# Performance work log

Hardware: AMD Instinct MI355X
Metric: run time of the kernel (lower is better)

## Reference

```python
import jax, jax.numpy as jnp
import numpy as np

RADIUS = 1.0
NSAMPLE = 8
GROUPS = 8
EPS = 1e-5


def setup_inputs() -> dict:
    key = jax.random.key(0)
    ks = jax.random.split(key, 8)
    b, n_p, dim, C = 4, 4096, 128, 64
    coords = jax.random.normal(ks[0], (b, n_p, 3), jnp.float32)
    xyz2 = jax.random.normal(ks[1], (b, n_p, 3), jnp.float32)
    fmap1 = jax.random.normal(ks[2], (b, dim, n_p), jnp.float32)
    fmap2 = jax.random.normal(ks[3], (b, dim, n_p), jnp.float32)
    conv_w = jax.random.normal(ks[4], (C, 4), jnp.float32) * 0.1
    conv_b = jnp.zeros((C,), jnp.float32)
    gn_gamma = jnp.ones((C,), jnp.float32)
    gn_beta = jnp.zeros((C,), jnp.float32)
    prelu_a = jnp.full((1,), 0.25, jnp.float32)
    out_w = jax.random.normal(ks[5], (C, C), jnp.float32) * 0.1
    out_b = jnp.zeros((C,), jnp.float32)
    return {"coords": coords, "xyz2": xyz2, "fmap1": fmap1, "fmap2": fmap2,
            "conv_w": conv_w, "conv_b": conv_b, "gn_gamma": gn_gamma,
            "gn_beta": gn_beta, "prelu_a": prelu_a, "out_w": out_w, "out_b": out_b}


def ball_query(xyz2, coords, radius, nsample):
    # first-nsample points of xyz2 within `radius` of each query in coords,
    # padded with the first valid index (0 if none) -- matches PointNet++ ball query.
    n = xyz2.shape[1]
    d2 = jnp.sum((coords[:, :, None, :] - xyz2[:, None, :, :]) ** 2, axis=-1)  # [b,m,n]
    j = jnp.arange(n, dtype=jnp.float32)
    score = jnp.where(d2 < radius * radius, -j, -float(n))  # larger score = earlier valid idx
    vals, _ = jax.lax.top_k(score, nsample)  # [b,m,nsample]
    valid = vals > -float(n)
    idx = (-vals).astype(jnp.int32)
    first = jnp.where(valid[..., :1], idx[..., :1], 0)
    return jnp.where(valid, idx, first)  # [b,m,nsample]


def reference(coords, xyz2, fmap1, fmap2, conv_w, conv_b, gn_gamma, gn_beta, prelu_a, out_w, out_b):
    b, n_p, _ = coords.shape
    dim = fmap1.shape[1]
    # corr = fmap1^T fmap2 / sqrt(dim): [b, n_p, n_p]
    corr = jnp.einsum('bdn,bdm->bnm', fmap1, fmap2) / jnp.sqrt(jnp.float32(dim))
    idx = ball_query(xyz2, coords, RADIUS, NSAMPLE)  # [b,n_p,nsample]
    # grouped_xyz: xyz2[idx] - coords -> [b, 3, n_p, nsample]
    gathered = jax.vmap(lambda pts, ind: pts[ind])(xyz2, idx)  # [b,n_p,ns,3]
    grouped_xyz = jnp.transpose(gathered - coords[:, :, None, :], (0, 3, 1, 2))
    # corr gather along source dim
    cur_corr = jnp.take_along_axis(corr, idx, axis=2)[:, None]  # [b,1,n_p,ns]
    feat = jnp.concatenate([cur_corr, grouped_xyz], axis=1)  # [b,4,n_p,ns]
    # 1x1 Conv2d
    x = jnp.einsum('oc,bcns->bons', conv_w, feat) + conv_b[None, :, None, None]
    # GroupNorm(8, 64)
    C = x.shape[1]
    xg = x.reshape(b, GROUPS, C // GROUPS, n_p, NSAMPLE)
    mu = jnp.mean(xg, axis=(2, 3, 4), keepdims=True)
    var = jnp.var(xg, axis=(2, 3, 4), keepdims=True)
    xg = (xg - mu) * jax.lax.rsqrt(var + EPS)
    x = xg.reshape(b, C, n_p, NSAMPLE) * gn_gamma[None, :, None, None] + gn_beta[None, :, None, None]
    # PReLU (single shared slope)
    x = jnp.where(x >= 0, x, prelu_a[0] * x)
    # max over neighbors
    x = jnp.max(x, axis=3)  # [b,64,n_p]
    # 1x1 Conv1d out
    return jnp.einsum('oc,bcn->bon', out_w, x) + out_b[None, :, None]
```

## Files before the change

kernel.cpp:

```cpp
#include <hip/hip_runtime.h>
#include <hip/hip_cooperative_groups.h>
#include <math.h>

namespace cg = cooperative_groups;

#define B 4
#define NP 4096
#define DIM 128
#define CCH 64
#define NS 8

struct SM {
  float4 fs4[128];
  int sidx[128];
  float4 ow4[1024];
  float cw[256];
  float cb[64], ob[64];
  union {
    float tile[128][35];
    struct { float As[16 * 132]; float red[4][14]; } k2;
    struct {
      float4 vs4[256];
      float Av[64], Bv[64], red2[8][14], Sm[14], SxA[64], SxxA[64];
    } k3;
  } u;
};

__global__ __launch_bounds__(256, 4) void fused_all(
    const float* __restrict__ coords, const float* __restrict__ xyz2,
    const float* __restrict__ f1, const float* __restrict__ f2,
    const float* __restrict__ conv_w, const float* __restrict__ conv_b,
    const float* __restrict__ gamma, const float* __restrict__ beta,
    const float* __restrict__ prelu, const float* __restrict__ out_w,
    const float* __restrict__ out_b, float* __restrict__ out,
    float* __restrict__ f2T, float* __restrict__ parts, int useT) {
  cg::grid_group grid = cg::this_grid();
  __shared__ SM sm;
  int blk = blockIdx.x;
  int t = threadIdx.x;
  int bq = (blk & 7) >> 1;
  int chunk = ((blk >> 3) << 1) | (blk & 1);
  int m0 = chunk * 16;

  if (useT) {
    int b = blk >> 8;
    int n0 = (blk & 255) * 16;
    const float* s = f2 + (size_t)b * DIM * NP;
    float* dd = f2T + (size_t)b * NP * DIM;
#pragma unroll
    for (int it = 0; it < 2; ++it) {
      int f = t + it * 256;
      int d = f >> 2, ng = f & 3;
      float4 v = *(const float4*)&s[(size_t)d * NP + n0 + ng * 4];
      *(float4*)&sm.u.tile[d][ng * 4 + (d >> 5)] = v;
    }
    __syncthreads();
#pragma unroll
    for (int it = 0; it < 2; ++it) {
      int f = t + it * 256;
      int n = f >> 5, dg = f & 31;
      int ar = dg >> 3;
      float4 w;
      w.x = sm.u.tile[dg * 4 + 0][n + ar];
      w.y = sm.u.tile[dg * 4 + 1][n + ar];
      w.z = sm.u.tile[dg * 4 + 2][n + ar];
      w.w = sm.u.tile[dg * 4 + 3][n + ar];
      *(float4*)&dd[(size_t)(n0 + n) * DIM + dg * 4] = w;
    }
  }

  {
    int wv = t >> 6, lane = t & 63;
    const float* xz = xyz2 + (size_t)bq * NP * 3;
    float cx[4], cy[4], cz[4];
#pragma unroll
    for (int qi = 0; qi < 4; ++qi) {
      const float* cp = coords + ((size_t)bq * NP + m0 + wv * 4 + qi) * 3;
      cx[qi] = cp[0]; cy[qi] = cp[1]; cz[qi] = cp[2];
    }
    int cnt[4] = {0, 0, 0, 0};
    int first[4] = {0, 0, 0, 0};
    int j0 = lane * 3;
    float ax = xz[j0], ay = xz[j0 + 1], az = xz[j0 + 2];
    int j1 = (64 + lane) * 3;
    float bx = xz[j1], by = xz[j1 + 1], bz = xz[j1 + 2];
#pragma unroll 1
    for (int c = 0; c < 64; c += 2) {
      int c2 = (c + 2 < 64) ? c + 2 : 63;
      int c3 = (c + 3 < 64) ? c + 3 : 63;
      int jn2 = (c2 * 64 + lane) * 3, jn3 = (c3 * 64 + lane) * 3;
      float nax = xz[jn2], nay = xz[jn2 + 1], naz = xz[jn2 + 2];
      float nbx = xz[jn3], nby = xz[jn3 + 1], nbz = xz[jn3 + 2];
#pragma unroll
      for (int qi = 0; qi < 4; ++qi) {
        if (cnt[qi] < NS) {
          float dx = __fsub_rn(cx[qi], ax);
          float dy = __fsub_rn(cy[qi], ay);
          float dz = __fsub_rn(cz[qi], az);
          float d2 = __fadd_rn(__fadd_rn(__fmul_rn(dx, dx), __fmul_rn(dy, dy)),
                               __fmul_rn(dz, dz));
          bool hit = d2 < 1.0f;
          unsigned long long mk = __ballot(hit);
          if (mk) {
            int rank = cnt[qi] + __popcll(mk & ((1ull << lane) - 1ull));
            if (hit && rank < NS)
              sm.sidx[(wv * 4 + qi) * NS + rank] = c * 64 + lane;
            if (cnt[qi] == 0) first[qi] = c * 64 + (__ffsll(mk) - 1);
            cnt[qi] += __popcll(mk);
          }
        }
      }
      if ((cnt[0] >= NS) & (cnt[1] >= NS) & (cnt[2] >= NS) & (cnt[3] >= NS))
        break;
#pragma unroll
      for (int qi = 0; qi < 4; ++qi) {
        if (cnt[qi] < NS) {
          float dx = __fsub_rn(cx[qi], bx);
          float dy = __fsub_rn(cy[qi], by);
          float dz = __fsub_rn(cz[qi], bz);
          float d2 = __fadd_rn(__fadd_rn(__fmul_rn(dx, dx), __fmul_rn(dy, dy)),
                               __fmul_rn(dz, dz));
          bool hit = d2 < 1.0f;
          unsigned long long mk = __ballot(hit);
          if (mk) {
            int rank = cnt[qi] + __popcll(mk & ((1ull << lane) - 1ull));
            if (hit && rank < NS)
              sm.sidx[(wv * 4 + qi) * NS + rank] = (c + 1) * 64 + lane;
            if (cnt[qi] == 0) first[qi] = (c + 1) * 64 + (__ffsll(mk) - 1);
            cnt[qi] += __popcll(mk);
          }
        }
      }
      if ((cnt[0] >= NS) & (cnt[1] >= NS) & (cnt[2] >= NS) & (cnt[3] >= NS))
        break;
      ax = nax; ay = nay; az = naz;
      bx = nbx; by = nby; bz = nbz;
    }
#pragma unroll
    for (int qi = 0; qi < 4; ++qi) {
      if (lane < NS && lane >= cnt[qi])
        sm.sidx[(wv * 4 + qi) * NS + lane] = first[qi];
    }
  }

  {
    const float4* src = (const float4*)out_w;
#pragma unroll
    for (int k = 0; k < 4; ++k) {
      int i4 = t + k * 256;
      int oo = i4 >> 4, gg = i4 & 15;
      sm.ow4[oo * 16 + (gg ^ ((oo >> 2) & 7))] = src[i4];
    }
    sm.cw[t] = conv_w[t];
    if (t < 64) {
      sm.cb[t] = conv_b[t];
      sm.ob[t] = out_b[t];
    }
  }

  grid.sync();

  {
    auto& k2 = sm.u.k2;
    int b = bq;
    int g = t >> 3;
    int l = t & 7;
    float pm[14];
#pragma unroll
    for (int k = 0; k < 14; ++k) pm[k] = 0.f;

    if (useT) {
      int id0 = sm.sidx[g], id1 = sm.sidx[32 + g];
      int id2 = sm.sidx[64 + g], id3 = sm.sidx[96 + g];
      const float4* br0 = (const float4*)(f2T + ((size_t)b * NP + id0) * DIM) + l;
      const float4* br1 = (const float4*)(f2T + ((size_t)b * NP + id1) * DIM) + l;
      const float4* br2 = (const float4*)(f2T + ((size_t)b * NP + id2) * DIM) + l;
      const float4* br3 = (const float4*)(f2T + ((size_t)b * NP + id3) * DIM) + l;
      float4 y00 = br0[0], y01 = br0[8], y02 = br0[16], y03 = br0[24];
      float4 y10 = br1[0], y11 = br1[8], y12 = br1[16], y13 = br1[24];
      const float* xq0 = xyz2 + ((size_t)b * NP + id0) * 3;
      const float* xq1 = xyz2 + ((size_t)b * NP + id1) * 3;
      float x0x = xq0[0], x0y = xq0[1], x0z = xq0[2];
      float x1x = xq1[0], x1y = xq1[1], x1z = xq1[2];

#pragma unroll
      for (int pass = 0; pass < 2; ++pass) {
        int d = pass * 64 + (t >> 2);
        int j4 = t & 3;
        float4 v = *(const float4*)&f1[(size_t)(b * DIM + d) * NP + m0 + j4 * 4];
        k2.As[(j4 * 4 + 0) * 132 + d] = v.x;
        k2.As[(j4 * 4 + 1) * 132 + d] = v.y;
        k2.As[(j4 * 4 + 2) * 132 + d] = v.z;
        k2.As[(j4 * 4 + 3) * 132 + d] = v.w;
      }
      __syncthreads();
      float4 y20 = br2[0], y21 = br2[8], y22 = br2[16], y23 = br2[24];
      float4 y30 = br3[0], y31 = br3[8], y32 = br3[16], y33 = br3[24];
      const float* xq2 = xyz2 + ((size_t)b * NP + id2) * 3;
      const float* xq3 = xyz2 + ((size_t)b * NP + id3) * 3;
      float x2x = xq2[0], x2y = xq2[1], x2z = xq2[2];
      float x3x = xq3[0], x3y = xq3[1], x3z = xq3[2];

#define DO_R(r, ya, yb, yc, yd, nxx, nxy, nxz)                                 \
      {                                                                        \
        int pi = (r) * 32 + g;                                                 \
        int m = pi >> 3;                                                       \
        const float4* arow = (const float4*)&k2.As[m * 132] + l;               \
        float4 a0 = arow[0], a1 = arow[8], a2 = arow[16], a3 = arow[24];       \
        float acc = a0.x * ya.x + a0.y * ya.y + a0.z * ya.z + a0.w * ya.w +    \
                    a1.x * yb.x + a1.y * yb.y + a1.z * yb.z + a1.w * yb.w +    \
                    a2.x * yc.x + a2.y * yc.y + a2.z * yc.z + a2.w * yc.w +    \
                    a3.x * yd.x + a3.y * yd.y + a3.z * yd.z + a3.w * yd.w;     \
        acc += __shfl_xor(acc, 1);                                             \
        acc += __shfl_xor(acc, 2);                                             \
        acc += __shfl_xor(acc, 4);                                             \
        float corr = acc * 0.08838834764831843f;                               \
        const float* cpq = coords + ((size_t)b * NP + m0 + m) * 3;             \
        float dx = nxx - cpq[0], dy = nxy - cpq[1], dz = nxz - cpq[2];         \
        if (l == 0) {                                                          \
          float4 fv;                                                           \
          fv.x = corr; fv.y = dx; fv.z = dy; fv.w = dz;                        \
          sm.fs4[pi] = fv;                                                     \
        }                                                                      \
        pm[0] += corr; pm[1] += dx; pm[2] += dy; pm[3] += dz;                  \
        pm[4] += corr * corr; pm[5] += corr * dx; pm[6] += corr * dy;          \
        pm[7] += corr * dz; pm[8] += dx * dx; pm[9] += dx * dy;                \
        pm[10] += dx * dz; pm[11] += dy * dy; pm[12] += dy * dz;               \
        pm[13] += dz * dz;                                                     \
      }
      DO_R(0, y00, y01, y02, y03, x0x, x0y, x0z)
      DO_R(1, y10, y11, y12, y13, x1x, x1y, x1z)
      DO_R(2, y20, y21, y22, y23, x2x, x2y, x2z)
      DO_R(3, y30, y31, y32, y33, x3x, x3y, x3z)
#undef DO_R
    } else {
      __syncthreads();
      int idv[4];
#pragma unroll
      for (int r = 0; r < 4; ++r) idv[r] = sm.sidx[r * 32 + g];
#pragma unroll
      for (int r = 0; r < 4; ++r) {
        int pi = r * 32 + g;
        int m = pi >> 3;
        int id = idv[r];
        float acc = 0.f;
#pragma unroll
        for (int k = 0; k < 4; ++k) {
#pragma unroll
          for (int c = 0; c < 4; ++c) {
            int d = (l + 8 * k) * 4 + c;
            acc += f1[(size_t)(b * DIM + d) * NP + m0 + m] *
                   f2[(size_t)(b * DIM + d) * NP + id];
          }
        }
        acc += __shfl_xor(acc, 1);
        acc += __shfl_xor(acc, 2);
        acc += __shfl_xor(acc, 4);
        float corr = acc * 0.08838834764831843f;
        const float* cpq = coords + ((size_t)b * NP + m0 + m) * 3;
        const float* xp = xyz2 + ((size_t)b * NP + id) * 3;
        float dx = xp[0] - cpq[0], dy = xp[1] - cpq[1], dz = xp[2] - cpq[2];
        if (l == 0) {
          float4 fv;
          fv.x = corr; fv.y = dx; fv.z = dy; fv.w = dz;
          sm.fs4[pi] = fv;
        }
        pm[0] += corr; pm[1] += dx; pm[2] += dy; pm[3] += dz;
        pm[4] += corr * corr; pm[5] += corr * dx; pm[6] += corr * dy;
        pm[7] += corr * dz; pm[8] += dx * dx; pm[9] += dx * dy;
        pm[10] += dx * dz; pm[11] += dy * dy; pm[12] += dy * dz;
        pm[13] += dz * dz;
      }
    }

#pragma unroll
    for (int k = 0; k < 14; ++k) {
      float v = pm[k];
#pragma unroll
      for (int off = 32; off; off >>= 1) v += __shfl_xor(v, off);
      pm[k] = v;
    }
    int lane = t & 63, wvv = t >> 6;
    if (lane == 0) {
#pragma unroll
      for (int k = 0; k < 14; ++k) k2.red[wvv][k] = pm[k];
    }
    __syncthreads();
    if (t < 14) {
      float ssum = (k2.red[0][t] + k2.red[1][t] + k2.red[2][t] + k2.red[3][t]) * 0.125f;
      parts[((size_t)bq * 256 + chunk) * 14 + t] = ssum;
    }
  }

  grid.sync();

  {
    auto& kb = sm.u.k3;
    int b = bq;
    int n0 = m0;
    if (t < 112) {
      int k = t % 14, jg = t / 14;
      float s = 0.f;
      const float* pp = parts + ((size_t)b * 256 + jg * 32) * 14 + k;
#pragma unroll 8
      for (int j = 0; j < 32; ++j) s += pp[j * 14];
      kb.red2[jg][k] = s;
    }
    float alpha = prelu[0];
    __syncthreads();
    if (t < 14) {
      float s = 0.f;
#pragma unroll
      for (int jg = 0; jg < 8; ++jg) s += kb.red2[jg][t];
      kb.Sm[t] = s;
    }
    __syncthreads();
    if (t < 64) {
      int o = t;
      float w0 = sm.cw[o * 4 + 0], w1 = sm.cw[o * 4 + 1];
      float w2 = sm.cw[o * 4 + 2], w3 = sm.cw[o * 4 + 3];
      float bo = sm.cb[o];
      const float cnt = (float)(NP * NS);
      float wS1 = w0 * kb.Sm[0] + w1 * kb.Sm[1] + w2 * kb.Sm[2] + w3 * kb.Sm[3];
      float q = w0 * w0 * kb.Sm[4] + w1 * w1 * kb.Sm[8] + w2 * w2 * kb.Sm[11] +
                w3 * w3 * kb.Sm[13] +
                2.f * (w0 * w1 * kb.Sm[5] + w0 * w2 * kb.Sm[6] + w0 * w3 * kb.Sm[7] +
                       w1 * w2 * kb.Sm[9] + w1 * w3 * kb.Sm[10] + w2 * w3 * kb.Sm[12]);
      kb.SxA[o] = wS1 + bo * cnt;
      kb.SxxA[o] = q + 2.f * bo * wS1 + bo * bo * cnt;
    }
    __syncthreads();
    if (t < 64) {
      int o = t, g = o >> 3;
      const float cnt = (float)(NP * NS);
      float sm_ = 0.f, s2 = 0.f;
#pragma unroll
      for (int k = 0; k < 8; ++k) {
        sm_ += kb.SxA[g * 8 + k];
        s2 += kb.SxxA[g * 8 + k];
      }
      float mean = sm_ / (cnt * 8.f);
      float e2 = s2 / (cnt * 8.f);
      float var = e2 - mean * mean;
      float inv = rsqrtf(var + 1e-5f);
      float A = gamma[o] * inv;
      kb.Av[o] = A;
      kb.Bv[o] = beta[o] - mean * A;
    }
    __syncthreads();

    {
      int o = t & 63;
      int pw = t >> 6;
      float w0 = sm.cw[o * 4 + 0], w1 = sm.cw[o * 4 + 1];
      float w2 = sm.cw[o * 4 + 2], w3 = sm.cw[o * 4 + 3];
      float A = kb.Av[o], Bc = kb.Bv[o], bb = sm.cb[o];
      float* vsf = (float*)kb.vs4;
#pragma unroll
      for (int i = 0; i < 4; ++i) {
        int p = pw * 4 + i;
        float mx = -INFINITY;
#pragma unroll
        for (int s = 0; s < NS; ++s) {
          float4 f = sm.fs4[p * 8 + s];
          float x = fmaf(w0, f.x, fmaf(w1, f.y, fmaf(w2, f.z, fmaf(w3, f.w, bb))));
          float y = fmaf(A, x, Bc);
          y = (y >= 0.f) ? y : alpha * y;
          mx = fmaxf(mx, y);
        }
        vsf[(p * 16 + ((o >> 2) ^ ((p >> 2) & 7))) * 4 + (o & 3)] = mx;
      }
    }
    __syncthreads();

    {
      int ti = t >> 3;
      int tj = t & 7;
      float acc[2][2];
#pragma unroll
      for (int oi = 0; oi < 2; ++oi)
#pragma unroll
        for (int pj = 0; pj < 2; ++pj) acc[oi][pj] = 0.f;
#pragma unroll
      for (int g = 0; g < 16; ++g) {
        float4 vv[2], ww[2];
#pragma unroll
        for (int pj = 0; pj < 2; ++pj) {
          int p = tj * 2 + pj;
          vv[pj] = kb.vs4[p * 16 + (g ^ ((p >> 2) & 7))];
        }
#pragma unroll
        for (int oi = 0; oi < 2; ++oi) {
          int oo = ti * 2 + oi;
          ww[oi] = sm.ow4[oo * 16 + (g ^ ((oo >> 2) & 7))];
        }
#pragma unroll
        for (int oi = 0; oi < 2; ++oi)
#pragma unroll
          for (int pj = 0; pj < 2; ++pj) {
            acc[oi][pj] = fmaf(ww[oi].x, vv[pj].x, acc[oi][pj]);
            acc[oi][pj] = fmaf(ww[oi].y, vv[pj].y, acc[oi][pj]);
            acc[oi][pj] = fmaf(ww[oi].z, vv[pj].z, acc[oi][pj]);
            acc[oi][pj] = fmaf(ww[oi].w, vv[pj].w, acc[oi][pj]);
          }
      }
#pragma unroll
      for (int oi = 0; oi < 2; ++oi) {
        int oo = ti * 2 + oi;
        float bb = sm.ob[oo];
        float2 r;
        r.x = acc[oi][0] + bb;
        r.y = acc[oi][1] + bb;
        *(float2*)&out[((size_t)b * CCH + oo) * NP + n0 + tj * 2] = r;
      }
    }
  }
}

__global__ __launch_bounds__(256) void kA_bq_transpose(
    const float* __restrict__ coords, const float* __restrict__ xyz2,
    int* __restrict__ idxb, const float* __restrict__ f2,
    float* __restrict__ o2) {
  int blk = blockIdx.x;
  int t = threadIdx.x;
  __shared__ float tile[128][33];
  if (blk < B * NP) {
    int b = blk >> 12, m = blk & (NP - 1);
    int wv = t >> 6, lane = t & 63;
    const float* cp = coords + ((size_t)b * NP + m) * 3;
    float cx = cp[0], cy = cp[1], cz = cp[2];
    const float* xz = xyz2 + (size_t)b * NP * 3;
    int base = wv * 1024;
    int j0 = (base + lane) * 3;
    float px = xz[j0], py = xz[j0 + 1], pz = xz[j0 + 2];
    int cnt = 0, myidx = 0;
    for (int c = 0; c < 16 && cnt < NS; ++c) {
      int cn = (c < 15) ? c + 1 : 15;
      int jn = (base + cn * 64 + lane) * 3;
      float nx = xz[jn], ny = xz[jn + 1], nz = xz[jn + 2];
      float dx = __fsub_rn(cx, px);
      float dy = __fsub_rn(cy, py);
      float dz = __fsub_rn(cz, pz);
      float d2 = __fadd_rn(__fadd_rn(__fmul_rn(dx, dx), __fmul_rn(dy, dy)),
                           __fmul_rn(dz, dz));
      unsigned long long mk = __ballot(d2 < 1.0f);
      while (mk && cnt < NS) {
        int bpos = __ffsll(mk) - 1;
        int jf = base + c * 64 + bpos;
        if (lane == cnt) myidx = jf;
        ++cnt;
        mk &= mk - 1;
      }
      px = nx; py = ny; pz = nz;
    }
    __shared__ int sidx[4][NS];
    __shared__ int scnt[4];
    if (lane < NS) sidx[wv][lane] = myidx;
    if (lane == 0) scnt[wv] = cnt;
    __syncthreads();
    if (t < NS) {
      int c0 = scnt[0], c1 = scnt[1], c2 = scnt[2], c3 = scnt[3];
      int total = c0 + c1 + c2 + c3;
      int v;
      if (t < c0) v = sidx[0][t];
      else if (t < c0 + c1) v = sidx[1][t - c0];
      else if (t < c0 + c1 + c2) v = sidx[2][t - c0 - c1];
      else if (t < total) v = sidx[3][t - c0 - c1 - c2];
      else v = (c0 > 0) ? sidx[0][0]
             : (c1 > 0) ? sidx[1][0]
             : (c2 > 0) ? sidx[2][0]
             : (c3 > 0) ? sidx[3][0] : 0;
      idxb[((size_t)b * NP + m) * NS + t] = v;
    }
  } else {
    int tb = blk - B * NP;
    int b = tb >> 7;
    int n0 = (tb & 127) * 32;
    const float* s = f2 + (size_t)b * DIM * NP;
    float* d = o2 + (size_t)b * NP * DIM;
    int dr = t >> 3;
    int ng = t & 7;
#pragma unroll
    for (int k = 0; k < 4; ++k) {
      int dd = dr + 32 * k;
      float4 v = *(const float4*)&s[(size_t)dd * NP + n0 + ng * 4];
      tile[dd][ng * 4 + 0] = v.x;
      tile[dd][ng * 4 + 1] = v.y;
      tile[dd][ng * 4 + 2] = v.z;
      tile[dd][ng * 4 + 3] = v.w;
    }
    __syncthreads();
    int n = t >> 3;
#pragma unroll
    for (int k = 0; k < 4; ++k) {
      int d0 = (t & 7) * 4 + 32 * k;
      float4 w;
      w.x = tile[d0 + 0][n];
      w.y = tile[d0 + 1][n];
      w.z = tile[d0 + 2][n];
      w.w = tile[d0 + 3][n];
      *(float4*)&d[(size_t)(n0 + n) * DIM + d0] = w;
    }
  }
}

__global__ __launch_bounds__(256) void k2_corrfeat(
    const float* __restrict__ f1, const float* __restrict__ f2T,
    const float* __restrict__ coords, const float* __restrict__ xyz2,
    const int* __restrict__ idxb, float* __restrict__ feat,
    float* __restrict__ parts, int trans) {
  int i = blockIdx.x;
  int b = (i & 7) >> 1;
  int chunk = ((i >> 3) << 1) | (i & 1);
  int m0 = chunk * 16;
  int t = threadIdx.x;
  __shared__ float As[16 * 132];
  __shared__ float red[4][14];
  if (trans) {
#pragma unroll
    for (int pass = 0; pass < 2; ++pass) {
      int d = pass * 64 + (t >> 2);
      int j4 = t & 3;
      float4 v = *(const float4*)&f1[(size_t)(b * DIM + d) * NP + m0 + j4 * 4];
      As[(j4 * 4 + 0) * 132 + d] = v.x;
      As[(j4 * 4 + 1) * 132 + d] = v.y;
      As[(j4 * 4 + 2) * 132 + d] = v.z;
      As[(j4 * 4 + 3) * 132 + d] = v.w;
    }
  }
  __syncthreads();
  int g = t >> 3;
  int l = t & 7;
  size_t ibase = ((size_t)b * NP + m0) * NS;
  int idv[4];
#pragma unroll
  for (int r = 0; r < 4; ++r) idv[r] = idxb[ibase + r * 32 + g];
  float pm[14];
#pragma unroll
  for (int k = 0; k < 14; ++k) pm[k] = 0.f;
#pragma unroll
  for (int r = 0; r < 4; ++r) {
    int pi = r * 32 + g;
    int m = pi >> 3, s = pi & 7;
    int id = idv[r];
    float acc = 0.f;
    if (trans) {
      const float4* brow = (const float4*)(f2T + ((size_t)b * NP + id) * DIM);
      const float4* arow = (const float4*)&As[m * 132];
#pragma unroll
      for (int k = 0; k < 4; ++k) {
        float4 y = brow[l + 8 * k];
        float4 x = arow[l + 8 * k];
        acc += x.x * y.x + x.y * y.y + x.z * y.z + x.w * y.w;
      }
    } else {
#pragma unroll
      for (int k = 0; k < 4; ++k) {
#pragma unroll
        for (int c = 0; c < 4; ++c) {
          int d = (l + 8 * k) * 4 + c;
          acc += f1[(size_t)(b * DIM + d) * NP + m0 + m] *
                 f2T[(size_t)(b * DIM + d) * NP + id];
        }
      }
    }
    acc += __shfl_xor(acc, 1);
    acc += __shfl_xor(acc, 2);
    acc += __shfl_xor(acc, 4);
    float corr = acc * 0.08838834764831843f;
    const float* cp = coords + ((size_t)b * NP + m0 + m) * 3;
    const float* xp = xyz2 + ((size_t)b * NP + id) * 3;
    float dx = xp[0] - cp[0], dy = xp[1] - cp[1], dz = xp[2] - cp[2];
    if (l == 0) {
      float4 fv;
      fv.x = corr; fv.y = dx; fv.z = dy; fv.w = dz;
      ((float4*)feat)[((size_t)b * NP + m0 + m) * NS + s] = fv;
    }
    pm[0] += corr; pm[1] += dx; pm[2] += dy; pm[3] += dz;
    pm[4] += corr * corr; pm[5] += corr * dx; pm[6] += corr * dy;
    pm[7] += corr * dz; pm[8] += dx * dx; pm[9] += dx * dy;
    pm[10] += dx * dz; pm[11] += dy * dy; pm[12] += dy * dz; pm[13] += dz * dz;
  }
#pragma unroll
  for (int k = 0; k < 14; ++k) {
    float v = pm[k];
#pragma unroll
    for (int off = 32; off; off >>= 1) v += __shfl_xor(v, off);
    pm[k] = v;
  }
  int lane = t & 63, wvv = t >> 6;
  if (lane == 0) {
#pragma unroll
    for (int k = 0; k < 14; ++k) red[wvv][k] = pm[k];
  }
  __syncthreads();
  if (t < 14) {
    float ssum = (red[0][t] + red[1][t] + red[2][t] + red[3][t]) * 0.125f;
    parts[((size_t)b * 256 + chunk) * 14 + t] = ssum;
  }
}

__global__ __launch_bounds__(256) void kB_out(
    const float* __restrict__ feat, const float* __restrict__ parts,
    const float* __restrict__ conv_w, const float* __restrict__ conv_b,
    const float* __restrict__ gamma, const float* __restrict__ beta,
    const float* __restrict__ prelu, const float* __restrict__ out_w,
    const float* __restrict__ out_b, float* __restrict__ out) {
  int b = blockIdx.x >> 8;
  int n0 = (blockIdx.x & 255) * 16;
  __shared__ float4 fs4[16 * 8];
  __shared__ float4 vs4[16 * 16];
  __shared__ float4 ow4[64 * 16];
  __shared__ float cw[256], cb_[64], Av[64], Bv[64], ob_[64];
  __shared__ float red2[8][14];
  __shared__ float Sm[14];
  __shared__ float SxA[64], SxxA[64];
  int t = threadIdx.x;
  if (t < 128) fs4[t] = ((const float4*)(feat + ((size_t)b * NP + n0) * 32))[t];
  {
    const float4* src = (const float4*)out_w;
#pragma unroll
    for (int k = 0; k < 4; ++k) {
      int i4 = t + k * 256;
      int oo = i4 >> 4, gg = i4 & 15;
      ow4[oo * 16 + (gg ^ ((oo >> 2) & 7))] = src[i4];
    }
  }
  cw[t] = conv_w[t];
  if (t < 64) {
    cb_[t] = conv_b[t];
    ob_[t] = out_b[t];
  }
  if (t < 112) {
    int k = t % 14, jg = t / 14;
    float s = 0.f;
    const float* pp = parts + ((size_t)b * 256 + jg * 32) * 14 + k;
    for (int j = 0; j < 32; ++j) s += pp[j * 14];
    red2[jg][k] = s;
  }
  float alpha = prelu[0];
  __syncthreads();
  if (t < 14) {
    float s = 0.f;
#pragma unroll
    for (int jg = 0; jg < 8; ++jg) s += red2[jg][t];
    Sm[t] = s;
  }
  __syncthreads();
  if (t < 64) {
    int o = t;
    float w0 = cw[o * 4 + 0], w1 = cw[o * 4 + 1];
    float w2 = cw[o * 4 + 2], w3 = cw[o * 4 + 3];
    float bo = cb_[o];
    const float cnt = (float)(NP * NS);
    float wS1 = w0 * Sm[0] + w1 * Sm[1] + w2 * Sm[2] + w3 * Sm[3];
    float q = w0 * w0 * Sm[4] + w1 * w1 * Sm[8] + w2 * w2 * Sm[11] +
              w3 * w3 * Sm[13] +
              2.f * (w0 * w1 * Sm[5] + w0 * w2 * Sm[6] + w0 * w3 * Sm[7] +
                     w1 * w2 * Sm[9] + w1 * w3 * Sm[10] + w2 * w3 * Sm[12]);
    SxA[o] = wS1 + bo * cnt;
    SxxA[o] = q + 2.f * bo * wS1 + bo * bo * cnt;
  }
  __syncthreads();
  if (t < 64) {
    int o = t, g = o >> 3;
    const float cnt = (float)(NP * NS);
    float sm = 0.f, s2 = 0.f;
#pragma unroll
    for (int k = 0; k < 8; ++k) {
// ... 65 lines not shown
    }
#pragma unroll
    for (int oi = 0; oi < 2; ++oi) {
      int oo = ti * 2 + oi;
      float bb = ob_[oo];
      float2 r;
      r.x = acc[oi][0] + bb;
      r.y = acc[oi][1] + bb;
      *(float2*)&out[((size_t)b * CCH + oo) * NP + n0 + tj * 2] = r;
    }
  }
}

extern "C" void kernel_launch(void* const* d_in, const int* in_sizes, int n_in,
                              void* d_out, int out_size, void* d_ws, size_t ws_size,
                              hipStream_t stream) {
  const float* coords = (const float*)d_in[0];
  const float* xyz2 = (const float*)d_in[1];
  const float* fmap1 = (const float*)d_in[2];
  const float* fmap2 = (const float*)d_in[3];
  const float* conv_w = (const float*)d_in[4];
  const float* conv_b = (const float*)d_in[5];
  const float* gamma = (const float*)d_in[6];
  const float* beta = (const float*)d_in[7];
  const float* prelu = (const float*)d_in[8];
  const float* out_w = (const float*)d_in[9];
  const float* out_b = (const float*)d_in[10];
  float* out = (float*)d_out;
  float* ws = (float*)d_ws;

  const size_t BND = (size_t)B * NP * DIM;
  const size_t FEAT = (size_t)B * NP * NS * 4;
  const size_t PARTS = (size_t)B * 256 * 14;
  size_t needT = (BND + FEAT + PARTS + 512) * sizeof(float) +
                 (size_t)B * NP * NS * sizeof(int);
  int useT = (ws_size >= needT) ? 1 : 0;

  float* f2T = ws;
  float* featp = useT ? (f2T + BND) : ws;
  float* parts = featp + FEAT;
  int* idxp = (int*)(parts + PARTS + 512);

  int maxBlocks = 0;
  hipError_t oe = hipOccupancyMaxActiveBlocksPerMultiprocessor(
      &maxBlocks, fused_all, 256, 0);
  if (oe == hipSuccess && maxBlocks >= 4) {
    void* args[] = {(void*)&coords, (void*)&xyz2,   (void*)&fmap1,
                    (void*)&fmap2,  (void*)&conv_w, (void*)&conv_b,
                    (void*)&gamma,  (void*)&beta,   (void*)&prelu,
                    (void*)&out_w,  (void*)&out_b,  (void*)&out,
                    (void*)&f2T,    (void*)&parts,  (void*)&useT};
    hipError_t le = hipLaunchCooperativeKernel(
        fused_all, dim3(1024), dim3(256), args, 0, stream);
    if (le == hipSuccess) return;
  }

  int nblk = B * NP + (useT ? (B * (NP / 32)) : 0);
  kA_bq_transpose<<<dim3(nblk), dim3(256), 0, stream>>>(coords, xyz2, idxp,
                                                        fmap2, f2T);
  k2_corrfeat<<<dim3(1024), dim3(256), 0, stream>>>(
      fmap1, useT ? f2T : fmap2, coords, xyz2, idxp, featp, parts, useT);
  kB_out<<<dim3(B * (NP / 16)), dim3(256), 0, stream>>>(
      featp, parts, conv_w, conv_b, gamma, beta, prelu, out_w, out_b, out);
}
```

Measured before the change: 50.35 us.

## Replace cooperative grid-sync kernel with three ordinary kernel launches

Splits the single cooperative kernel, which used two grid-wide syncs, into three ordinary launches: a transpose of fmap2, a kernel that fuses the ball query with the correlation and feature computation, and the existing output kernel. The aim is to drop the cost of grid barriers and the occupancy limit that cooperative launch imposes. The fused ball query also no longer writes neighbour indices to global memory. The cost is two extra launch boundaries, and the feature tensor now makes a round trip through global memory instead of staying in shared memory.

```diff
diff --git a/kernel.cpp b/kernel.cpp
--- a/kernel.cpp
+++ b/kernel.cpp
@@ -1,8 +1,5 @@
 #include <hip/hip_runtime.h>
-#include <hip/hip_cooperative_groups.h>
 #include <math.h>
-
-namespace cg = cooperative_groups;
 
 #define B 4
 #define NP 4096
@@ -10,62 +7,64 @@
 #define CCH 64
 #define NS 8
 
-struct SM {
-  float4 fs4[128];
-  int sidx[128];
-  float4 ow4[1024];
-  float cw[256];
-  float cb[64], ob[64];
-  union {
-    float tile[128][35];
-    struct { float As[16 * 132]; float red[4][14]; } k2;
-    struct {
-      float4 vs4[256];
-      float Av[64], Bv[64], red2[8][14], Sm[14], SxA[64], SxxA[64];
-    } k3;
-  } u;
-};
-
-__global__ __launch_bounds__(256, 4) void fused_all(
+__global__ __launch_bounds__(256) void k_transpose(
+    const float* __restrict__ f2, float* __restrict__ o2) {
+  int tb = blockIdx.x;
+  int t = threadIdx.x;
+  __shared__ float tile[128][33];
+  int b = tb >> 7;
+  int n0 = (tb & 127) * 32;
+  const float* s = f2 + (size_t)b * DIM * NP;
+  float* d = o2 + (size_t)b * NP * DIM;
+  int dr = t >> 3;
+  int ng = t & 7;
+#pragma unroll
+  for (int k = 0; k < 4; ++k) {
+    int dd = dr + 32 * k;
+    float4 v = *(const float4*)&s[(size_t)dd * NP + n0 + ng * 4];
+    tile[dd][ng * 4 + 0] = v.x;
+    tile[dd][ng * 4 + 1] = v.y;
+    tile[dd][ng * 4 + 2] = v.z;
+    tile[dd][ng * 4 + 3] = v.w;
+  }
+  __syncthreads();
+  int n = t >> 3;
+#pragma unroll
+  for (int k = 0; k < 4; ++k) {
+    int d0 = (t & 7) * 4 + 32 * k;
+    float4 w;
+    w.x = tile[d0 + 0][n];
+    w.y = tile[d0 + 1][n];
+    w.z = tile[d0 + 2][n];
+    w.w = tile[d0 + 3][n];
+    *(float4*)&d[(size_t)(n0 + n) * DIM + d0] = w;
+  }
+}
+
+__global__ __launch_bounds__(256) void k_bqcorr(
     const float* __restrict__ coords, const float* __restrict__ xyz2,
     const float* __restrict__ f1, const float* __restrict__ f2,
-    const float* __restrict__ conv_w, const float* __restrict__ conv_b,
-    const float* __restrict__ gamma, const float* __restrict__ beta,
-    const float* __restrict__ prelu, const float* __restrict__ out_w,
-    const float* __restrict__ out_b, float* __restrict__ out,
-    float* __restrict__ f2T, float* __restrict__ parts, int useT) {
-  cg::grid_group grid = cg::this_grid();
-  __shared__ SM sm;
+    const float* __restrict__ f2T, float* __restrict__ feat,
+    float* __restrict__ parts, int trans) {
   int blk = blockIdx.x;
   int t = threadIdx.x;
   int bq = (blk & 7) >> 1;
   int chunk = ((blk >> 3) << 1) | (blk & 1);
   int m0 = chunk * 16;
-
-  if (useT) {
-    int b = blk >> 8;
-    int n0 = (blk & 255) * 16;
-    const float* s = f2 + (size_t)b * DIM * NP;
-    float* dd = f2T + (size_t)b * NP * DIM;
-#pragma unroll
-    for (int it = 0; it < 2; ++it) {
-      int f = t + it * 256;
-      int d = f >> 2, ng = f & 3;
-      float4 v = *(const float4*)&s[(size_t)d * NP + n0 + ng * 4];
-      *(float4*)&sm.u.tile[d][ng * 4 + (d >> 5)] = v;
-    }
-    __syncthreads();
-#pragma unroll
-    for (int it = 0; it < 2; ++it) {
-      int f = t + it * 256;
-      int n = f >> 5, dg = f & 31;
-      int ar = dg >> 3;
-      float4 w;
-      w.x = sm.u.tile[dg * 4 + 0][n + ar];
-      w.y = sm.u.tile[dg * 4 + 1][n + ar];
-      w.z = sm.u.tile[dg * 4 + 2][n + ar];
-      w.w = sm.u.tile[dg * 4 + 3][n + ar];
-      *(float4*)&dd[(size_t)(n0 + n) * DIM + dg * 4] = w;
+  __shared__ float As[16 * 132];
+  __shared__ int sidx[128];
+  __shared__ float red[4][14];
+
+  if (trans) {
+#pragma unroll
+    for (int pass = 0; pass < 2; ++pass) {
+      int d = pass * 64 + (t >> 2);
+      int j4 = t & 3;
+      float4 v = *(const float4*)&f1[(size_t)(bq * DIM + d) * NP + m0 + j4 * 4];
+      As[(j4 * 4 + 0) * 132 + d] = v.x;
+      As[(j4 * 4 + 1) * 132 + d] = v.y;
+      As[(j4 * 4 + 2) * 132 + d] = v.z;
+      As[(j4 * 4 + 3) * 132 + d] = v.w;
     }
   }
 
@@ -104,7 +103,7 @@
           if (mk) {
             int rank = cnt[qi] + __popcll(mk & ((1ull << lane) - 1ull));
             if (hit && rank < NS)
-              sm.sidx[(wv * 4 + qi) * NS + rank] = c * 64 + lane;
+              sidx[(wv * 4 + qi) * NS + rank] = c * 64 + lane;
             if (cnt[qi] == 0) first[qi] = c * 64 + (__ffsll(mk) - 1);
             cnt[qi] += __popcll(mk);
           }
@@ -125,7 +124,7 @@
           if (mk) {
             int rank = cnt[qi] + __popcll(mk & ((1ull << lane) - 1ull));
             if (hit && rank < NS)
-              sm.sidx[(wv * 4 + qi) * NS + rank] = (c + 1) * 64 + lane;
+              sidx[(wv * 4 + qi) * NS + rank] = (c + 1) * 64 + lane;
             if (cnt[qi] == 0) first[qi] = (c + 1) * 64 + (__ffsll(mk) - 1);
             cnt[qi] += __popcll(mk);
           }
@@ -139,448 +138,109 @@
 #pragma unroll
     for (int qi = 0; qi < 4; ++qi) {
       if (lane < NS && lane >= cnt[qi])
-        sm.sidx[(wv * 4 + qi) * NS + lane] = first[qi];
-    }
-  }
-
-  {
-    const float4* src = (const float4*)out_w;
-#pragma unroll
-    for (int k = 0; k < 4; ++k) {
-      int i4 = t + k * 256;
-      int oo = i4 >> 4, gg = i4 & 15;
-      sm.ow4[oo * 16 + (gg ^ ((oo >> 2) & 7))] = src[i4];
-    }
-    sm.cw[t] = conv_w[t];
-    if (t < 64) {
-      sm.cb[t] = conv_b[t];
-      sm.ob[t] = out_b[t];
-    }
-  }
-
-  grid.sync();
-
-  {
-    auto& k2 = sm.u.k2;
-    int b = bq;
-    int g = t >> 3;
-    int l = t & 7;
-    float pm[14];
-#pragma unroll
-    for (int k = 0; k < 14; ++k) pm[k] = 0.f;
-
-    if (useT) {
-      int id0 = sm.sidx[g], id1 = sm.sidx[32 + g];
-      int id2 = sm.sidx[64 + g], id3 = sm.sidx[96 + g];
-      const float4* br0 = (const float4*)(f2T + ((size_t)b * NP + id0) * DIM) + l;
-      const float4* br1 = (const float4*)(f2T + ((size_t)b * NP + id1) * DIM) + l;
-      const float4* br2 = (const float4*)(f2T + ((size_t)b * NP + id2) * DIM) + l;
-      const float4* br3 = (const float4*)(f2T + ((size_t)b * NP + id3) * DIM) + l;
-      float4 y00 = br0[0], y01 = br0[8], y02 = br0[16], y03 = br0[24];
-      float4 y10 = br1[0], y11 = br1[8], y12 = br1[16], y13 = br1[24];
-      const float* xq0 = xyz2 + ((size_t)b * NP + id0) * 3;
-      const float* xq1 = xyz2 + ((size_t)b * NP + id1) * 3;
-      float x0x = xq0[0], x0y = xq0[1], x0z = xq0[2];
-      float x1x = xq1[0], x1y = xq1[1], x1z = xq1[2];
-
-#pragma unroll
-      for (int pass = 0; pass < 2; ++pass) {
-        int d = pass * 64 + (t >> 2);
-        int j4 = t & 3;
-        float4 v = *(const float4*)&f1[(size_t)(b * DIM + d) * NP + m0 + j4 * 4];
-        k2.As[(j4 * 4 + 0) * 132 + d] = v.x;
-        k2.As[(j4 * 4 + 1) * 132 + d] = v.y;
-        k2.As[(j4 * 4 + 2) * 132 + d] = v.z;
-        k2.As[(j4 * 4 + 3) * 132 + d] = v.w;
-      }
-      __syncthreads();
-      float4 y20 = br2[0], y21 = br2[8], y22 = br2[16], y23 = br2[24];
-      float4 y30 = br3[0], y31 = br3[8], y32 = br3[16], y33 = br3[24];
-      const float* xq2 = xyz2 + ((size_t)b * NP + id2) * 3;
-      const float* xq3 = xyz2 + ((size_t)b * NP + id3) * 3;
-      float x2x = xq2[0], x2y = xq2[1], x2z = xq2[2];
-      float x3x = xq3[0], x3y = xq3[1], x3z = xq3[2];
-
-#define DO_R(r, ya, yb, yc, yd, nxx, nxy, nxz)                                 \
-      {                                                                        \
-        int pi = (r) * 32 + g;                                                 \
-        int m = pi >> 3;                                                       \
-        const float4* arow = (const float4*)&k2.As[m * 132] + l;               \
-        float4 a0 = arow[0], a1 = arow[8], a2 = arow[16], a3 = arow[24];       \
-        float acc = a0.x * ya.x + a0.y * ya.y + a0.z * ya.z + a0.w * ya.w +    \
-                    a1.x * yb.x + a1.y * yb.y + a1.z * yb.z + a1.w * yb.w +    \
-                    a2.x * yc.x + a2.y * yc.y + a2.z * yc.z + a2.w * yc.w +    \
-                    a3.x * yd.x + a3.y * yd.y + a3.z * yd.z + a3.w * yd.w;     \
-        acc += __shfl_xor(acc, 1);                                             \
-        acc += __shfl_xor(acc, 2);                                             \
-        acc += __shfl_xor(acc, 4);                                             \
-        float corr = acc * 0.08838834764831843f;                               \
-        const float* cpq = coords + ((size_t)b * NP + m0 + m) * 3;             \
-        float dx = nxx - cpq[0], dy = nxy - cpq[1], dz = nxz - cpq[2];         \
-        if (l == 0) {                                                          \
-          float4 fv;                                                           \
-          fv.x = corr; fv.y = dx; fv.z = dy; fv.w = dz;                        \
-          sm.fs4[pi] = fv;                                                     \
-        }                                                                      \
-        pm[0] += corr; pm[1] += dx; pm[2] += dy; pm[3] += dz;                  \
-        pm[4] += corr * corr; pm[5] += corr * dx; pm[6] += corr * dy;          \
-        pm[7] += corr * dz; pm[8] += dx * dx; pm[9] += dx * dy;                \
-        pm[10] += dx * dz; pm[11] += dy * dy; pm[12] += dy * dz;               \
-        pm[13] += dz * dz;                                                     \
-      }
-      DO_R(0, y00, y01, y02, y03, x0x, x0y, x0z)
-      DO_R(1, y10, y11, y12, y13, x1x, x1y, x1z)
-      DO_R(2, y20, y21, y22, y23, x2x, x2y, x2z)
-      DO_R(3, y30, y31, y32, y33, x3x, x3y, x3z)
-#undef DO_R
-    } else {
-      __syncthreads();
-      int idv[4];
-#pragma unroll
-      for (int r = 0; r < 4; ++r) idv[r] = sm.sidx[r * 32 + g];
-#pragma unroll
-      for (int r = 0; r < 4; ++r) {
-        int pi = r * 32 + g;
-        int m = pi >> 3;
-        int id = idv[r];
-        float acc = 0.f;
-#pragma unroll
-        for (int k = 0; k < 4; ++k) {
-#pragma unroll
-          for (int c = 0; c < 4; ++c) {
-            int d = (l + 8 * k) * 4 + c;
-            acc += f1[(size_t)(b * DIM + d) * NP + m0 + m] *
-                   f2[(size_t)(b * DIM + d) * NP + id];
-          }
-        }
-        acc += __shfl_xor(acc, 1);
-        acc += __shfl_xor(acc, 2);
-        acc += __shfl_xor(acc, 4);
-        float corr = acc * 0.08838834764831843f;
-        const float* cpq = coords + ((size_t)b * NP + m0 + m) * 3;
-        const float* xp = xyz2 + ((size_t)b * NP + id) * 3;
-        float dx = xp[0] - cpq[0], dy = xp[1] - cpq[1], dz = xp[2] - cpq[2];
-        if (l == 0) {
-          float4 fv;
-          fv.x = corr; fv.y = dx; fv.z = dy; fv.w = dz;
-          sm.fs4[pi] = fv;
-        }
-        pm[0] += corr; pm[1] += dx; pm[2] += dy; pm[3] += dz;
-        pm[4] += corr * corr; pm[5] += corr * dx; pm[6] += corr * dy;
-        pm[7] += corr * dz; pm[8] += dx * dx; pm[9] += dx * dy;
-        pm[10] += dx * dz; pm[11] += dy * dy; pm[12] += dy * dz;
-        pm[13] += dz * dz;
-      }
-    }
-
-#pragma unroll
-    for (int k = 0; k < 14; ++k) {
-      float v = pm[k];
-#pragma unroll
-      for (int off = 32; off; off >>= 1) v += __shfl_xor(v, off);
-      pm[k] = v;
-    }
-    int lane = t & 63, wvv = t >> 6;
-    if (lane == 0) {
-#pragma unroll
-      for (int k = 0; k < 14; ++k) k2.red[wvv][k] = pm[k];
-    }
-    __syncthreads();
-    if (t < 14) {
-      float ssum = (k2.red[0][t] + k2.red[1][t] + k2.red[2][t] + k2.red[3][t]) * 0.125f;
-      parts[((size_t)bq * 256 + chunk) * 14 + t] = ssum;
-    }
-  }
-
-  grid.sync();
-
-  {
-    auto& kb = sm.u.k3;
-    int b = bq;
-    int n0 = m0;
-    if (t < 112) {
-      int k = t % 14, jg = t / 14;
-      float s = 0.f;
-      const float* pp = parts + ((size_t)b * 256 + jg * 32) * 14 + k;
-#pragma unroll 8
-      for (int j = 0; j < 32; ++j) s += pp[j * 14];
-      kb.red2[jg][k] = s;
-    }
-    float alpha = prelu[0];
-    __syncthreads();
-    if (t < 14) {
-      float s = 0.f;
-#pragma unroll
-      for (int jg = 0; jg < 8; ++jg) s += kb.red2[jg][t];
-      kb.Sm[t] = s;
-    }
-    __syncthreads();
-    if (t < 64) {
-      int o = t;
-      float w0 = sm.cw[o * 4 + 0], w1 = sm.cw[o * 4 + 1];
-      float w2 = sm.cw[o * 4 + 2], w3 = sm.cw[o * 4 + 3];
-      float bo = sm.cb[o];
-      const float cnt = (float)(NP * NS);
-      float wS1 = w0 * kb.Sm[0] + w1 * kb.Sm[1] + w2 * kb.Sm[2] + w3 * kb.Sm[3];
-      float q = w0 * w0 * kb.Sm[4] + w1 * w1 * kb.Sm[8] + w2 * w2 * kb.Sm[11] +
-                w3 * w3 * kb.Sm[13] +
-                2.f * (w0 * w1 * kb.Sm[5] + w0 * w2 * kb.Sm[6] + w0 * w3 * kb.Sm[7] +
-                       w1 * w2 * kb.Sm[9] + w1 * w3 * kb.Sm[10] + w2 * w3 * kb.Sm[12]);
-      kb.SxA[o] = wS1 + bo * cnt;
-      kb.SxxA[o] = q + 2.f * bo * wS1 + bo * bo * cnt;
-    }
-    __syncthreads();
-    if (t < 64) {
-      int o = t, g = o >> 3;
-      const float cnt = (float)(NP * NS);
-      float sm_ = 0.f, s2 = 0.f;
-#pragma unroll
-      for (int k = 0; k < 8; ++k) {
-        sm_ += kb.SxA[g * 8 + k];
-        s2 += kb.SxxA[g * 8 + k];
-      }
-      float mean = sm_ / (cnt * 8.f);
-      float e2 = s2 / (cnt * 8.f);
-      float var = e2 - mean * mean;
-      float inv = rsqrtf(var + 1e-5f);
-      float A = gamma[o] * inv;
-      kb.Av[o] = A;
-      kb.Bv[o] = beta[o] - mean * A;
-    }
-    __syncthreads();
-
-    {
-      int o = t & 63;
-      int pw = t >> 6;
-      float w0 = sm.cw[o * 4 + 0], w1 = sm.cw[o * 4 + 1];
-      float w2 = sm.cw[o * 4 + 2], w3 = sm.cw[o * 4 + 3];
-      float A = kb.Av[o], Bc = kb.Bv[o], bb = sm.cb[o];
-      float* vsf = (float*)kb.vs4;
-#pragma unroll
-      for (int i = 0; i < 4; ++i) {
-        int p = pw * 4 + i;
-        float mx = -INFINITY;
-#pragma unroll
-        for (int s = 0; s < NS; ++s) {
-          float4 f = sm.fs4[p * 8 + s];
-          float x = fmaf(w0, f.x, fmaf(w1, f.y, fmaf(w2, f.z, fmaf(w3, f.w, bb))));
-          float y = fmaf(A, x, Bc);
-          y = (y >= 0.f) ? y : alpha * y;
-          mx = fmaxf(mx, y);
-        }
-        vsf[(p * 16 + ((o >> 2) ^ ((p >> 2) & 7))) * 4 + (o & 3)] = mx;
-      }
-    }
-    __syncthreads();
-
-    {
-      int ti = t >> 3;
-      int tj = t & 7;
-      float acc[2][2];
-#pragma unroll
-      for (int oi = 0; oi < 2; ++oi)
-#pragma unroll
-        for (int pj = 0; pj < 2; ++pj) acc[oi][pj] = 0.f;
-#pragma unroll
-      for (int g = 0; g < 16; ++g) {
-        float4 vv[2], ww[2];
-#pragma unroll
-        for (int pj = 0; pj < 2; ++pj) {
-          int p = tj * 2 + pj;
-          vv[pj] = kb.vs4[p * 16 + (g ^ ((p >> 2) & 7))];
-        }
-#pragma unroll
-        for (int oi = 0; oi < 2; ++oi) {
-          int oo = ti * 2 + oi;
-          ww[oi] = sm.ow4[oo * 16 + (g ^ ((oo >> 2) & 7))];
-        }
-#pragma unroll
-        for (int oi = 0; oi < 2; ++oi)
-#pragma unroll
-          for (int pj = 0; pj < 2; ++pj) {
-            acc[oi][pj] = fmaf(ww[oi].x, vv[pj].x, acc[oi][pj]);
-            acc[oi][pj] = fmaf(ww[oi].y, vv[pj].y, acc[oi][pj]);
-            acc[oi][pj] = fmaf(ww[oi].z, vv[pj].z, acc[oi][pj]);
-            acc[oi][pj] = fmaf(ww[oi].w, vv[pj].w, acc[oi][pj]);
-          }
-      }
-#pragma unroll
-      for (int oi = 0; oi < 2; ++oi) {
-        int oo = ti * 2 + oi;
-        float bb = sm.ob[oo];
-        float2 r;
-        r.x = acc[oi][0] + bb;
-        r.y = acc[oi][1] + bb;
-        *(float2*)&out[((size_t)b * CCH + oo) * NP + n0 + tj * 2] = r;
-      }
-    }
-  }
-}
-
-__global__ __launch_bounds__(256) void kA_bq_transpose(
-    const float* __restrict__ coords, const float* __restrict__ xyz2,
-    int* __restrict__ idxb, const float* __restrict__ f2,
-    float* __restrict__ o2) {
-  int blk = blockIdx.x;
-  int t = threadIdx.x;
-  __shared__ float tile[128][33];
-  if (blk < B * NP) {
-    int b = blk >> 12, m = blk & (NP - 1);
-    int wv = t >> 6, lane = t & 63;
-    const float* cp = coords + ((size_t)b * NP + m) * 3;
-    float cx = cp[0], cy = cp[1], cz = cp[2];
-    const float* xz = xyz2 + (size_t)b * NP * 3;
-    int base = wv * 1024;
-    int j0 = (base + lane) * 3;
-    float px = xz[j0], py = xz[j0 + 1], pz = xz[j0 + 2];
-    int cnt = 0, myidx = 0;
-    for (int c = 0; c < 16 && cnt < NS; ++c) {
-      int cn = (c < 15) ? c + 1 : 15;
-      int jn = (base + cn * 64 + lane) * 3;
-      float nx = xz[jn], ny = xz[jn + 1], nz = xz[jn + 2];
-      float dx = __fsub_rn(cx, px);
-      float dy = __fsub_rn(cy, py);
-      float dz = __fsub_rn(cz, pz);
-      float d2 = __fadd_rn(__fadd_rn(__fmul_rn(dx, dx), __fmul_rn(dy, dy)),
-                           __fmul_rn(dz, dz));
-      unsigned long long mk = __ballot(d2 < 1.0f);
-      while (mk && cnt < NS) {
-        int bpos = __ffsll(mk) - 1;
-        int jf = base + c * 64 + bpos;
-        if (lane == cnt) myidx = jf;
-        ++cnt;
-        mk &= mk - 1;
-      }
-      px = nx; py = ny; pz = nz;
-    }
-    __shared__ int sidx[4][NS];
-    __shared__ int scnt[4];
-    if (lane < NS) sidx[wv][lane] = myidx;
-    if (lane == 0) scnt[wv] = cnt;
-    __syncthreads();
-    if (t < NS) {
-      int c0 = scnt[0], c1 = scnt[1], c2 = scnt[2], c3 = scnt[3];
-      int total = c0 + c1 + c2 + c3;
-      int v;
-      if (t < c0) v = sidx[0][t];
-      else if (t < c0 + c1) v = sidx[1][t - c0];
-      else if (t < c0 + c1 + c2) v = sidx[2][t - c0 - c1];
-      else if (t < total) v = sidx[3][t - c0 - c1 - c2];
-      else v = (c0 > 0) ? sidx[0][0]
-             : (c1 > 0) ? sidx[1][0]
-             : (c2 > 0) ? sidx[2][0]
-             : (c3 > 0) ? sidx[3][0] : 0;
-      idxb[((size_t)b * NP + m) * NS + t] = v;
-    }
-  } else {
-    int tb = blk - B * NP;
-    int b = tb >> 7;
-    int n0 = (tb & 127) * 32;
-    const float* s = f2 + (size_t)b * DIM * NP;
-    float* d = o2 + (size_t)b * NP * DIM;
-    int dr = t >> 3;
-    int ng = t & 7;
-#pragma unroll
-    for (int k = 0; k < 4; ++k) {
-      int dd = dr + 32 * k;
-      float4 v = *(const float4*)&s[(size_t)dd * NP + n0 + ng * 4];
-      tile[dd][ng * 4 + 0] = v.x;
-      tile[dd][ng * 4 + 1] = v.y;
-      tile[dd][ng * 4 + 2] = v.z;
-      tile[dd][ng * 4 + 3] = v.w;
-    }
-    __syncthreads();
-    int n = t >> 3;
-#pragma unroll
-    for (int k = 0; k < 4; ++k) {
-      int d0 = (t & 7) * 4 + 32 * k;
-      float4 w;
-      w.x = tile[d0 + 0][n];
-      w.y = tile[d0 + 1][n];
-      w.z = tile[d0 + 2][n];
-      w.w = tile[d0 + 3][n];
-      *(float4*)&d[(size_t)(n0 + n) * DIM + d0] = w;
-    }
-  }
-}
-
-__global__ __launch_bounds__(256) void k2_corrfeat(
-    const float* __restrict__ f1, const float* __restrict__ f2T,
-    const float* __restrict__ coords, const float* __restrict__ xyz2,
-    const int* __restrict__ idxb, float* __restrict__ feat,
-    float* __restrict__ parts, int trans) {
-  int i = blockIdx.x;
-  int b = (i & 7) >> 1;
-  int chunk = ((i >> 3) << 1) | (i & 1);
-  int m0 = chunk * 16;
-  int t = threadIdx.x;
-  __shared__ float As[16 * 132];
-  __shared__ float red[4][14];
-  if (trans) {
-#pragma unroll
-    for (int pass = 0; pass < 2; ++pass) {
-      int d = pass * 64 + (t >> 2);
-      int j4 = t & 3;
-      float4 v = *(const float4*)&f1[(size_t)(b * DIM + d) * NP + m0 + j4 * 4];
-      As[(j4 * 4 + 0) * 132 + d] = v.x;
-      As[(j4 * 4 + 1) * 132 + d] = v.y;
-      As[(j4 * 4 + 2) * 132 + d] = v.z;
-      As[(j4 * 4 + 3) * 132 + d] = v.w;
-    }
-  }
-  __syncthreads();
+        sidx[(wv * 4 + qi) * NS + lane] = first[qi];
+    }
+  }
+  __syncthreads();
+
   int g = t >> 3;
   int l = t & 7;
-  size_t ibase = ((size_t)b * NP + m0) * NS;
-  int idv[4];
-#pragma unroll
-  for (int r = 0; r < 4; ++r) idv[r] = idxb[ibase + r * 32 + g];
   float pm[14];
 #pragma unroll
   for (int k = 0; k < 14; ++k) pm[k] = 0.f;
-#pragma unroll
-  for (int r = 0; r < 4; ++r) {
-    int pi = r * 32 + g;
-    int m = pi >> 3, s = pi & 7;
-    int id = idv[r];
-    float acc = 0.f;
-    if (trans) {
-      const float4* brow = (const float4*)(f2T + ((size_t)b * NP + id) * DIM);
-      const float4* arow = (const float4*)&As[m * 132];
-#pragma unroll
-      for (int k = 0; k < 4; ++k) {
-        float4 y = brow[l + 8 * k];
-        float4 x = arow[l + 8 * k];
-        acc += x.x * y.x + x.y * y.y + x.z * y.z + x.w * y.w;
-      }
-    } else {
+
+  if (trans) {
+    int id0 = sidx[g], id1 = sidx[32 + g];
+    int id2 = sidx[64 + g], id3 = sidx[96 + g];
+    const float4* br0 = (const float4*)(f2T + ((size_t)bq * NP + id0) * DIM) + l;
+    const float4* br1 = (const float4*)(f2T + ((size_t)bq * NP + id1) * DIM) + l;
+    const float4* br2 = (const float4*)(f2T + ((size_t)bq * NP + id2) * DIM) + l;
+    const float4* br3 = (const float4*)(f2T + ((size_t)bq * NP + id3) * DIM) + l;
+    float4 y00 = br0[0], y01 = br0[8], y02 = br0[16], y03 = br0[24];
+    float4 y10 = br1[0], y11 = br1[8], y12 = br1[16], y13 = br1[24];
+    const float* xq0 = xyz2 + ((size_t)bq * NP + id0) * 3;
+    const float* xq1 = xyz2 + ((size_t)bq * NP + id1) * 3;
+    float x0x = xq0[0], x0y = xq0[1], x0z = xq0[2];
+    float x1x = xq1[0], x1y = xq1[1], x1z = xq1[2];
+    float4 y20 = br2[0], y21 = br2[8], y22 = br2[16], y23 = br2[24];
+    float4 y30 = br3[0], y31 = br3[8], y32 = br3[16], y33 = br3[24];
+    const float* xq2 = xyz2 + ((size_t)bq * NP + id2) * 3;
+    const float* xq3 = xyz2 + ((size_t)bq * NP + id3) * 3;
+    float x2x = xq2[0], x2y = xq2[1], x2z = xq2[2];
+    float x3x = xq3[0], x3y = xq3[1], x3z = xq3[2];
+    size_t fbase = ((size_t)bq * NP + m0) * NS;
+
+#define DO_R(r, ya, yb, yc, yd, nxx, nxy, nxz)                                 \
+    {                                                                          \
+      int pi = (r) * 32 + g;                                                   \
+      int m = pi >> 3;                                                         \
+      const float4* arow = (const float4*)&As[m * 132] + l;                    \
+      float4 a0 = arow[0], a1 = arow[8], a2 = arow[16], a3 = arow[24];         \
+      float acc = a0.x * ya.x + a0.y * ya.y + a0.z * ya.z + a0.w * ya.w +      \
+                  a1.x * yb.x + a1.y * yb.y + a1.z * yb.z + a1.w * yb.w +      \
+                  a2.x * yc.x + a2.y * yc.y + a2.z * yc.z + a2.w * yc.w +      \
+                  a3.x * yd.x + a3.y * yd.y + a3.z * yd.z + a3.w * yd.w;       \
+      acc += __shfl_xor(acc, 1);                                               \
+      acc += __shfl_xor(acc, 2);                                               \
+      acc += __shfl_xor(acc, 4);                                               \
+      float corr = acc * 0.08838834764831843f;                                 \
+      const float* cpq = coords + ((size_t)bq * NP + m0 + m) * 3;              \
+      float dx = nxx - cpq[0], dy = nxy - cpq[1], dz = nxz - cpq[2];           \
+      if (l == 0) {                                                            \
+        float4 fv;                                                             \
+        fv.x = corr; fv.y = dx; fv.z = dy; fv.w = dz;                          \
+        ((float4*)feat)[fbase + pi] = fv;                                      \
+      }                                                                        \
+      pm[0] += corr; pm[1] += dx; pm[2] += dy; pm[3] += dz;                    \
+      pm[4] += corr * corr; pm[5] += corr * dx; pm[6] += corr * dy;            \
+      pm[7] += corr * dz; pm[8] += dx * dx; pm[9] += dx * dy;                  \
+      pm[10] += dx * dz; pm[11] += dy * dy; pm[12] += dy * dz;                 \
+      pm[13] += dz * dz;                                                       \
+    }
+    DO_R(0, y00, y01, y02, y03, x0x, x0y, x0z)
+    DO_R(1, y10, y11, y12, y13, x1x, x1y, x1z)
+    DO_R(2, y20, y21, y22, y23, x2x, x2y, x2z)
+    DO_R(3, y30, y31, y32, y33, x3x, x3y, x3z)
+#undef DO_R
+  } else {
+    int idv[4];
+#pragma unroll
+    for (int r = 0; r < 4; ++r) idv[r] = sidx[r * 32 + g];
+#pragma unroll
+    for (int r = 0; r < 4; ++r) {
+      int pi = r * 32 + g;
+      int m = pi >> 3, s = pi & 7;
+      int id = idv[r];
+      float acc = 0.f;
 #pragma unroll
       for (int k = 0; k < 4; ++k) {
 #pragma unroll
         for (int c = 0; c < 4; ++c) {
           int d = (l + 8 * k) * 4 + c;
-          acc += f1[(size_t)(b * DIM + d) * NP + m0 + m] *
-                 f2T[(size_t)(b * DIM + d) * NP + id];
+          acc += f1[(size_t)(bq * DIM + d) * NP + m0 + m] *
+                 f2[(size_t)(bq * DIM + d) * NP + id];
         }
       }
-    }
-    acc += __shfl_xor(acc, 1);
-    acc += __shfl_xor(acc, 2);
-    acc += __shfl_xor(acc, 4);
-    float corr = acc * 0.08838834764831843f;
-    const float* cp = coords + ((size_t)b * NP + m0 + m) * 3;
-    const float* xp = xyz2 + ((size_t)b * NP + id) * 3;
-    float dx = xp[0] - cp[0], dy = xp[1] - cp[1], dz = xp[2] - cp[2];
-    if (l == 0) {
-      float4 fv;
-      fv.x = corr; fv.y = dx; fv.z = dy; fv.w = dz;
-      ((float4*)feat)[((size_t)b * NP + m0 + m) * NS + s] = fv;
-    }
-    pm[0] += corr; pm[1] += dx; pm[2] += dy; pm[3] += dz;
-    pm[4] += corr * corr; pm[5] += corr * dx; pm[6] += corr * dy;
-    pm[7] += corr * dz; pm[8] += dx * dx; pm[9] += dx * dy;
-    pm[10] += dx * dz; pm[11] += dy * dy; pm[12] += dy * dz; pm[13] += dz * dz;
-  }
+      acc += __shfl_xor(acc, 1);
+      acc += __shfl_xor(acc, 2);
+      acc += __shfl_xor(acc, 4);
+      float corr = acc * 0.08838834764831843f;
+      const float* cpq = coords + ((size_t)bq * NP + m0 + m) * 3;
+      const float* xp = xyz2 + ((size_t)bq * NP + id) * 3;
+      float dx = xp[0] - cpq[0], dy = xp[1] - cpq[1], dz = xp[2] - cpq[2];
+      if (l == 0) {
+        float4 fv;
+        fv.x = corr; fv.y = dx; fv.z = dy; fv.w = dz;
+        ((float4*)feat)[((size_t)bq * NP + m0 + m) * NS + s] = fv;
+      }
+      pm[0] += corr; pm[1] += dx; pm[2] += dy; pm[3] += dz;
+      pm[4] += corr * corr; pm[5] += corr * dx; pm[6] += corr * dy;
+      pm[7] += corr * dz; pm[8] += dx * dx; pm[9] += dx * dy;
+      pm[10] += dx * dz; pm[11] += dy * dy; pm[12] += dy * dz;
+      pm[13] += dz * dz;
+    }
+  }
+
 #pragma unroll
   for (int k = 0; k < 14; ++k) {
     float v = pm[k];
@@ -596,7 +256,7 @@
   __syncthreads();
   if (t < 14) {
     float ssum = (red[0][t] + red[1][t] + red[2][t] + red[3][t]) * 0.125f;
-    parts[((size_t)b * 256 + chunk) * 14 + t] = ssum;
+    parts[((size_t)bq * 256 + chunk) * 14 + t] = ssum;
   }
 }
 
@@ -635,6 +295,7 @@
     int k = t % 14, jg = t / 14;
     float s = 0.f;
     const float* pp = parts + ((size_t)b * 256 + jg * 32) * 14 + k;
+#pragma unroll 8
     for (int j = 0; j < 32; ++j) s += pp[j * 14];
     red2[jg][k] = s;
   }
@@ -766,34 +427,17 @@
   const size_t BND = (size_t)B * NP * DIM;
   const size_t FEAT = (size_t)B * NP * NS * 4;
   const size_t PARTS = (size_t)B * 256 * 14;
-  size_t needT = (BND + FEAT + PARTS + 512) * sizeof(float) +
-                 (size_t)B * NP * NS * sizeof(int);
+  size_t needT = (BND + FEAT + PARTS + 512) * sizeof(float);
   int useT = (ws_size >= needT) ? 1 : 0;
 
   float* f2T = ws;
   float* featp = useT ? (f2T + BND) : ws;
   float* parts = featp + FEAT;
-  int* idxp = (int*)(parts + PARTS + 512);
-
-  int maxBlocks = 0;
-  hipError_t oe = hipOccupancyMaxActiveBlocksPerMultiprocessor(
-      &maxBlocks, fused_all, 256, 0);
-  if (oe == hipSuccess && maxBlocks >= 4) {
-    void* args[] = {(void*)&coords, (void*)&xyz2,   (void*)&fmap1,
-                    (void*)&fmap2,  (void*)&conv_w, (void*)&conv_b,
-                    (void*)&gamma,  (void*)&beta,   (void*)&prelu,
-                    (void*)&out_w,  (void*)&out_b,  (void*)&out,
-                    (void*)&f2T,    (void*)&parts,  (void*)&useT};
-    hipError_t le = hipLaunchCooperativeKernel(
-        fused_all, dim3(1024), dim3(256), args, 0, stream);
-    if (le == hipSuccess) return;
-  }
-
-  int nblk = B * NP + (useT ? (B * (NP / 32)) : 0);
-  kA_bq_transpose<<<dim3(nblk), dim3(256), 0, stream>>>(coords, xyz2, idxp,
-                                                        fmap2, f2T);
-  k2_corrfeat<<<dim3(1024), dim3(256), 0, stream>>>(
-      fmap1, useT ? f2T : fmap2, coords, xyz2, idxp, featp, parts, useT);
+
+  if (useT)
+    k_transpose<<<dim3(B * (NP / 32)), dim3(256), 0, stream>>>(fmap2, f2T);
+  k_bqcorr<<<dim3(1024), dim3(256), 0, stream>>>(
+      coords, xyz2, fmap1, fmap2, f2T, featp, parts, useT);
   kB_out<<<dim3(B * (NP / 16)), dim3(256), 0, stream>>>(
       featp, parts, conv_w, conv_b, gamma, beta, prelu, out_w, out_b, out);
 }
```

New measurement: 41.22 us, median of 2. 1.22x faster.
